# Optimization experiments

Measured on AMD Instinct MI355X. Metric: run time of the kernel, lower is better.

The kernel has to match this reference:

```python
import jax, jax.numpy as jnp
import numpy as np

B, H, T, D = 4, 16, 4096, 64
N_TASKS, K_LEN = 8, 128


def setup_inputs() -> dict:
    key = jax.random.key(0)
    ks = jax.random.split(key, 6)
    x = jax.random.normal(ks[0], (B, H, T, D), dtype=jnp.float32)
    q = jax.random.normal(ks[1], (B, H, T, D), dtype=jnp.float32)
    kv_k = jax.random.normal(ks[2], (N_TASKS, H, K_LEN, D), dtype=jnp.float32)
    kv_v = jax.random.normal(ks[3], (N_TASKS, H, K_LEN, D), dtype=jnp.float32)
    gates = jax.random.uniform(ks[4], (N_TASKS,), dtype=jnp.float32)
    trk_id = jax.random.randint(ks[5], (B, T), 0, N_TASKS, dtype=jnp.int64)
    return {"x": x, "q": q, "kv_k": kv_k, "kv_v": kv_v, "gates": gates, "trk_id": trk_id}


def reference(x, q, kv_k, kv_v, gates, trk_id):
    # Faithful to ICLAdaptor.fn: per-task SDPA of each token's query against
    # that task's (k, v) adaptor memory, scaled by a learned gate, scattered
    # back by trk_id, residual-added to x. Ragged torch gather/scatter is
    # expressed as masked per-task dense attention (small fixed n_tasks loop).
    d = q.shape[-1]
    scale = jnp.asarray(1.0, q.dtype) / jnp.sqrt(jnp.asarray(d, q.dtype))
    n_tasks = kv_k.shape[0]
    dx = jnp.zeros_like(q)
    for i in range(n_tasks):
        # scores: [b, h, t, k_len]
        s = jnp.einsum('bhtd,hkd->bhtk', q, kv_k[i]) * scale
        a = jax.nn.softmax(s, axis=-1)
        o = jnp.einsum('bhtk,hkd->bhtd', a, kv_v[i]) * gates[i]
        mask = (trk_id == i)[:, None, :, None]  # [b,1,t,1]
        dx = dx + jnp.where(mask, o, jnp.zeros((), o.dtype))
    return x + dx
```

## Files before the change

kernel.cpp:

```cpp
#include <hip/hip_runtime.h>

#define B_   4
#define H_   16
#define T_   4096
#define D_   64
#define KL_  128
#define NT_  8
#define NTOK (B_ * T_)
#define CAP  4096

typedef __bf16 bf16;
typedef __attribute__((ext_vector_type(8))) __bf16 bf16x8;
typedef __attribute__((ext_vector_type(4))) __bf16 bf16x4;
typedef __attribute__((ext_vector_type(4))) float  floatx4;


__global__ void zero_counts_k(int* __restrict__ ws) {
    if (threadIdx.x < NT_) ws[threadIdx.x] = 0;
}

__global__ void scatter_tokens_k(const int* __restrict__ trk, int* __restrict__ ws) {
    int* counts = ws;
    int* bucket = ws + NT_;
    int idx  = blockIdx.x * blockDim.x + threadIdx.x;
    int lane = threadIdx.x & 63;
    int task = (idx < NTOK) ? trk[idx] : -1;
    unsigned long long mymask = 0ull;
    int myCnt = 0;
#pragma unroll
    for (int i = 0; i < NT_; i++) {
        unsigned long long m = __ballot(task == i);
        if (task == i) mymask = m;
        if (lane == i) myCnt = (int)__popcll(m);
    }
    int b0 = 0;
    if (lane < NT_) b0 = atomicAdd(&counts[lane], myCnt);
    int myBase = __shfl(b0, (task < 0) ? 0 : task);
    if (idx < NTOK) {
        int pos = myBase + (int)__popcll(mymask & ((1ull << lane) - 1ull));
        bucket[task * CAP + pos] = idx;
    }
}

__global__ __launch_bounds__(256) void attn_k(
    const float* __restrict__ q,   const float* __restrict__ kvk,
    const float* __restrict__ kvv, const float* __restrict__ gates,
    const float* __restrict__ x,   float* __restrict__ out,
    const int* __restrict__ ws)
{
    __shared__ bf16 Kl[KL_ * 72];
    __shared__ bf16 Vt[D_ * 136];
    __shared__ bf16 Pl[4][16 * 136];

    const int task = blockIdx.z, h = blockIdx.y, chunk = blockIdx.x;
    const int cnt = ws[task];
    if (cnt == 0) return;
    const int* bucket = ws + NT_ + task * CAP;
    const float gate = gates[task];

    {
        const size_t kvbase = (size_t)(task * H_ + h) * (KL_ * D_ / 4);
        const float4* kf = (const float4*)kvk + kvbase;
        const float4* vf = (const float4*)kvv + kvbase;
        for (int ii = threadIdx.x; ii < KL_ * D_ / 4; ii += 256) {
            int k = ii >> 4, d4 = ii & 15;
            float4 a = kf[ii];
            bf16x4 w; w[0]=(bf16)a.x; w[1]=(bf16)a.y; w[2]=(bf16)a.z; w[3]=(bf16)a.w;
            *(bf16x4*)&Kl[k * 72 + d4 * 4] = w;
            float4 v = vf[ii];
            int d = d4 * 4;
            Vt[(d+0)*136 + k] = (bf16)v.x;
            Vt[(d+1)*136 + k] = (bf16)v.y;
            Vt[(d+2)*136 + k] = (bf16)v.z;
            Vt[(d+3)*136 + k] = (bf16)v.w;
        }
    }
    __syncthreads();

    const int wave = threadIdx.x >> 6;
    const int lane = threadIdx.x & 63;
    const int c = lane & 15, quad = lane >> 4;
    bf16* Pw = &Pl[wave][0];

    for (int ts = chunk * 4 + wave; ts * 16 < cnt; ts += 32) {
        int slotc = ts * 16 + c;
        int tokc  = bucket[slotc < cnt ? slotc : cnt - 1];
        int bb = tokc >> 12, tt = tokc & (T_ - 1);
        const float4* qf = (const float4*)q + ((size_t)((bb * H_ + h) * T_ + tt) * (D_ / 4));
        bf16x8 aq[2];
#pragma unroll
        for (int dc = 0; dc < 2; dc++) {
            float4 f0 = qf[dc * 8 + quad * 2];
            float4 f1 = qf[dc * 8 + quad * 2 + 1];
            aq[dc][0]=(bf16)f0.x; aq[dc][1]=(bf16)f0.y; aq[dc][2]=(bf16)f0.z; aq[dc][3]=(bf16)f0.w;
            aq[dc][4]=(bf16)f1.x; aq[dc][5]=(bf16)f1.y; aq[dc][6]=(bf16)f1.z; aq[dc][7]=(bf16)f1.w;
        }
        floatx4 sc[8];
#pragma unroll
        for (int nt = 0; nt < 8; nt++) {
            floatx4 z = {0.f, 0.f, 0.f, 0.f};
            sc[nt] = z;
#pragma unroll
            for (int dc = 0; dc < 2; dc++) {
                bf16x8 bk = *(const bf16x8*)&Kl[(nt * 16 + c) * 72 + dc * 32 + quad * 8];
                sc[nt] = __builtin_amdgcn_mfma_f32_16x16x32_bf16(aq[dc], bk, sc[nt], 0, 0, 0);
            }
        }
        float mx[4], lsum[4];
#pragma unroll
        for (int r = 0; r < 4; r++) {
            float m = -1e30f;
#pragma unroll
            for (int nt = 0; nt < 8; nt++) m = fmaxf(m, sc[nt][r]);
#pragma unroll
            for (int off = 1; off < 16; off <<= 1) m = fmaxf(m, __shfl_xor(m, off));
            mx[r] = m;
        }
#pragma unroll
        for (int r = 0; r < 4; r++) {
            float sum = 0.f;
#pragma unroll
            for (int nt = 0; nt < 8; nt++) {
                float p = exp2f((sc[nt][r] - mx[r]) * 0.18033688011112042f);
                sc[nt][r] = p;
                sum += p;
            }
#pragma unroll
            for (int off = 1; off < 16; off <<= 1) sum += __shfl_xor(sum, off);
            lsum[r] = sum;
        }
#pragma unroll
        for (int nt = 0; nt < 8; nt++)
#pragma unroll
            for (int r = 0; r < 4; r++)
                Pw[(quad * 4 + r) * 136 + nt * 16 + c] = (bf16)sc[nt][r];
        floatx4 acc[4];
#pragma unroll
        for (int dt = 0; dt < 4; dt++) { floatx4 z = {0.f,0.f,0.f,0.f}; acc[dt] = z; }
#pragma unroll
        for (int kc = 0; kc < 4; kc++) {
            bf16x8 ap = *(const bf16x8*)&Pw[c * 136 + kc * 32 + quad * 8];
#pragma unroll
            for (int dt = 0; dt < 4; dt++) {
                bf16x8 bv = *(const bf16x8*)&Vt[(dt * 16 + c) * 136 + kc * 32 + quad * 8];
                acc[dt] = __builtin_amdgcn_mfma_f32_16x16x32_bf16(ap, bv, acc[dt], 0, 0, 0);
            }
        }
#pragma unroll
        for (int r = 0; r < 4; r++) {
            int slot = ts * 16 + quad * 4 + r;
            if (slot < cnt) {
                int tok = bucket[slot];
                int b2 = tok >> 12, t2 = tok & (T_ - 1);
                float scale = gate / lsum[r];
                int base = ((b2 * H_ + h) * T_ + t2) * D_;
#pragma unroll
                for (int dt = 0; dt < 4; dt++) {
                    int off = base + dt * 16 + c;
                    out[off] = x[off] + acc[dt][r] * scale;
                }
            }
        }
    }
}

extern "C" void kernel_launch(void* const* d_in, const int* in_sizes, int n_in,
                              void* d_out, int out_size, void* d_ws, size_t ws_size,
                              hipStream_t stream) {
    const float* x     = (const float*)d_in[0];
    const float* q     = (const float*)d_in[1];
    const float* kvk   = (const float*)d_in[2];
    const float* kvv   = (const float*)d_in[3];
    const float* gates = (const float*)d_in[4];
    const int*   trk   = (const int*)d_in[5];
    float* out = (float*)d_out;
    int* ws = (int*)d_ws;

    zero_counts_k<<<1, 64, 0, stream>>>(ws);
    scatter_tokens_k<<<NTOK / 256, 256, 0, stream>>>(trk, ws);
    attn_k<<<dim3(8, H_, NT_), 256, 0, stream>>>(q, kvk, kvv, gates, x, out, ws);
}
```

Measured before the change: 239.9 us.

## Keep softmax probabilities in registers via shuffles and XOR-swizzle K/V LDS layout

Computes S transposed (K as the A operand) so each lane owns one token's scores. Softmax reductions then need only two cross-quad shuffles, and the P tile is rebuilt as the MFMA A operand through register shuffles instead of a per-wave LDS round trip. K and V^T in LDS switch from padded rows to XOR-swizzled unpadded rows to avoid bank conflicts. Other changes: x is prefetched before the matmuls, bucket reloads are replaced with shuffles, s_setprio is raised around the MFMA sections, and launch bounds now request 4 blocks per CU. The shuffle-based operand assembly adds VALU and cross-lane traffic in exchange for less LDS traffic and fewer syncs.

After: 271.1 us. +13.0%, slower.

```diff
diff --git a/kernel.cpp b/kernel.cpp
--- a/kernel.cpp
+++ b/kernel.cpp
@@ -13,7 +13,7 @@
 typedef __attribute__((ext_vector_type(8))) __bf16 bf16x8;
 typedef __attribute__((ext_vector_type(4))) __bf16 bf16x4;
 typedef __attribute__((ext_vector_type(4))) float  floatx4;
-
+typedef __attribute__((ext_vector_type(4))) unsigned int uint4v;
 
 __global__ void zero_counts_k(int* __restrict__ ws) {
     if (threadIdx.x < NT_) ws[threadIdx.x] = 0;
@@ -42,15 +42,20 @@
     }
 }
 
-__global__ __launch_bounds__(256) void attn_k(
+static __device__ __forceinline__ unsigned pk_bf16(float a, float b) {
+    unsigned short ua = __builtin_bit_cast(unsigned short, (bf16)a);
+    unsigned short ub = __builtin_bit_cast(unsigned short, (bf16)b);
+    return (unsigned)ua | ((unsigned)ub << 16);
+}
+
+__global__ __launch_bounds__(256, 4) void attn_k(
     const float* __restrict__ q,   const float* __restrict__ kvk,
     const float* __restrict__ kvv, const float* __restrict__ gates,
     const float* __restrict__ x,   float* __restrict__ out,
     const int* __restrict__ ws)
 {
-    __shared__ bf16 Kl[KL_ * 72];
-    __shared__ bf16 Vt[D_ * 136];
-    __shared__ bf16 Pl[4][16 * 136];
+    __shared__ bf16 Kl[KL_ * D_];
+    __shared__ bf16 Vt[D_ * KL_];
 
     const int task = blockIdx.z, h = blockIdx.y, chunk = blockIdx.x;
     const int cnt = ws[task];
@@ -62,102 +67,137 @@
         const size_t kvbase = (size_t)(task * H_ + h) * (KL_ * D_ / 4);
         const float4* kf = (const float4*)kvk + kvbase;
         const float4* vf = (const float4*)kvv + kvbase;
-        for (int ii = threadIdx.x; ii < KL_ * D_ / 4; ii += 256) {
+#pragma unroll
+        for (int it = 0; it < 8; it++) {
+            int ii = it * 256 + threadIdx.x;
             int k = ii >> 4, d4 = ii & 15;
             float4 a = kf[ii];
             bf16x4 w; w[0]=(bf16)a.x; w[1]=(bf16)a.y; w[2]=(bf16)a.z; w[3]=(bf16)a.w;
-            *(bf16x4*)&Kl[k * 72 + d4 * 4] = w;
+            *(bf16x4*)&Kl[(k << 6) + (((d4 >> 1) ^ (k & 7)) << 3) + ((d4 & 1) << 2)] = w;
             float4 v = vf[ii];
-            int d = d4 * 4;
-            Vt[(d+0)*136 + k] = (bf16)v.x;
-            Vt[(d+1)*136 + k] = (bf16)v.y;
-            Vt[(d+2)*136 + k] = (bf16)v.z;
-            Vt[(d+3)*136 + k] = (bf16)v.w;
+            int d0 = d4 << 2, ku = k >> 3, kl = k & 7;
+            Vt[(d0+0)*128 + ((ku ^ ((d0+0)&7))<<3) + kl] = (bf16)v.x;
+            Vt[(d0+1)*128 + ((ku ^ ((d0+1)&7))<<3) + kl] = (bf16)v.y;
+            Vt[(d0+2)*128 + ((ku ^ ((d0+2)&7))<<3) + kl] = (bf16)v.z;
+            Vt[(d0+3)*128 + ((ku ^ ((d0+3)&7))<<3) + kl] = (bf16)v.w;
         }
     }
     __syncthreads();
 
+    const int lane = threadIdx.x & 63;
     const int wave = threadIdx.x >> 6;
-    const int lane = threadIdx.x & 63;
     const int c = lane & 15, quad = lane >> 4;
-    bf16* Pw = &Pl[wave][0];
+    const int cswz = c & 7;
+    const int src_h0 = c + 16 * (( 2 * quad     ) & 3);
+    const int src_h1 = c + 16 * (( 2 * quad + 1 ) & 3);
+    const bool hiSel = ((quad >> 1) & 1) != 0;
 
     for (int ts = chunk * 4 + wave; ts * 16 < cnt; ts += 32) {
-        int slotc = ts * 16 + c;
-        int tokc  = bucket[slotc < cnt ? slotc : cnt - 1];
-        int bb = tokc >> 12, tt = tokc & (T_ - 1);
-        const float4* qf = (const float4*)q + ((size_t)((bb * H_ + h) * T_ + tt) * (D_ / 4));
+        const int slotc = ts * 16 + c;
+        const int tokc  = bucket[slotc < cnt ? slotc : cnt - 1];
+
         bf16x8 aq[2];
+        {
+            int bb = tokc >> 12, tt = tokc & (T_ - 1);
+            const float4* qf = (const float4*)q + ((size_t)((bb * H_ + h) * T_ + tt) * (D_ / 4));
+#pragma unroll
+            for (int dc = 0; dc < 2; dc++) {
+                float4 f0 = qf[dc * 8 + quad * 2];
+                float4 f1 = qf[dc * 8 + quad * 2 + 1];
+                aq[dc][0]=(bf16)f0.x; aq[dc][1]=(bf16)f0.y; aq[dc][2]=(bf16)f0.z; aq[dc][3]=(bf16)f0.w;
+                aq[dc][4]=(bf16)f1.x; aq[dc][5]=(bf16)f1.y; aq[dc][6]=(bf16)f1.z; aq[dc][7]=(bf16)f1.w;
+            }
+        }
+
+        float xr[4][4];
+        int base_r[4];
+#pragma unroll
+        for (int r = 0; r < 4; r++) {
+            int tok = __shfl(tokc, quad * 4 + r);
+            int b2 = tok >> 12, t2 = tok & (T_ - 1);
+            base_r[r] = ((b2 * H_ + h) * T_ + t2) * D_;
+            if (ts * 16 + quad * 4 + r < cnt) {
+#pragma unroll
+                for (int dt = 0; dt < 4; dt++) xr[r][dt] = x[base_r[r] + dt * 16 + c];
+            }
+        }
+
+        floatx4 sc[8];
+#pragma unroll
+        for (int nt = 0; nt < 8; nt++) { floatx4 z = {0.f,0.f,0.f,0.f}; sc[nt] = z; }
+        __builtin_amdgcn_s_setprio(1);
 #pragma unroll
         for (int dc = 0; dc < 2; dc++) {
-            float4 f0 = qf[dc * 8 + quad * 2];
-            float4 f1 = qf[dc * 8 + quad * 2 + 1];
-            aq[dc][0]=(bf16)f0.x; aq[dc][1]=(bf16)f0.y; aq[dc][2]=(bf16)f0.z; aq[dc][3]=(bf16)f0.w;
-            aq[dc][4]=(bf16)f1.x; aq[dc][5]=(bf16)f1.y; aq[dc][6]=(bf16)f1.z; aq[dc][7]=(bf16)f1.w;
-        }
-        floatx4 sc[8];
-#pragma unroll
-        for (int nt = 0; nt < 8; nt++) {
-            floatx4 z = {0.f, 0.f, 0.f, 0.f};
-            sc[nt] = z;
-#pragma unroll
-            for (int dc = 0; dc < 2; dc++) {
-                bf16x8 bk = *(const bf16x8*)&Kl[(nt * 16 + c) * 72 + dc * 32 + quad * 8];
-                sc[nt] = __builtin_amdgcn_mfma_f32_16x16x32_bf16(aq[dc], bk, sc[nt], 0, 0, 0);
-            }
-        }
-        float mx[4], lsum[4];
-#pragma unroll
-        for (int r = 0; r < 4; r++) {
-            float m = -1e30f;
-#pragma unroll
-            for (int nt = 0; nt < 8; nt++) m = fmaxf(m, sc[nt][r]);
-#pragma unroll
-            for (int off = 1; off < 16; off <<= 1) m = fmaxf(m, __shfl_xor(m, off));
-            mx[r] = m;
-        }
-#pragma unroll
-        for (int r = 0; r < 4; r++) {
-            float sum = 0.f;
 #pragma unroll
             for (int nt = 0; nt < 8; nt++) {
-                float p = exp2f((sc[nt][r] - mx[r]) * 0.18033688011112042f);
+                bf16x8 ak = *(const bf16x8*)&Kl[((nt * 16 + c) << 6) + (((4 * dc + quad) ^ cswz) << 3)];
+                sc[nt] = __builtin_amdgcn_mfma_f32_16x16x32_bf16(ak, aq[dc], sc[nt], 0, 0, 0);
+            }
+        }
+        __builtin_amdgcn_s_setprio(0);
+
+        float m = -1e30f;
+#pragma unroll
+        for (int nt = 0; nt < 8; nt++)
+#pragma unroll
+            for (int r = 0; r < 4; r++) m = fmaxf(m, sc[nt][r]);
+        m = fmaxf(m, __shfl_xor(m, 16));
+        m = fmaxf(m, __shfl_xor(m, 32));
+        float sum = 0.f;
+#pragma unroll
+        for (int nt = 0; nt < 8; nt++)
+#pragma unroll
+            for (int r = 0; r < 4; r++) {
+                float p = exp2f((sc[nt][r] - m) * 0.18033688011112042f);
                 sc[nt][r] = p;
                 sum += p;
             }
-#pragma unroll
-            for (int off = 1; off < 16; off <<= 1) sum += __shfl_xor(sum, off);
-            lsum[r] = sum;
-        }
-#pragma unroll
-        for (int nt = 0; nt < 8; nt++)
-#pragma unroll
-            for (int r = 0; r < 4; r++)
-                Pw[(quad * 4 + r) * 136 + nt * 16 + c] = (bf16)sc[nt][r];
+        sum += __shfl_xor(sum, 16);
+        sum += __shfl_xor(sum, 32);
+        float ginv = gate / sum;
+
+        unsigned pkv[8][2];
+#pragma unroll
+        for (int nt = 0; nt < 8; nt++) {
+            pkv[nt][0] = pk_bf16(sc[nt][0], sc[nt][1]);
+            pkv[nt][1] = pk_bf16(sc[nt][2], sc[nt][3]);
+        }
+
         floatx4 acc[4];
 #pragma unroll
         for (int dt = 0; dt < 4; dt++) { floatx4 z = {0.f,0.f,0.f,0.f}; acc[dt] = z; }
 #pragma unroll
         for (int kc = 0; kc < 4; kc++) {
-            bf16x8 ap = *(const bf16x8*)&Pw[c * 136 + kc * 32 + quad * 8];
+            unsigned e0 = pkv[2*kc][0],   e1 = pkv[2*kc][1];
+            unsigned o0 = pkv[2*kc+1][0], o1 = pkv[2*kc+1][1];
+            unsigned a0e = __shfl(e0, src_h0), a0o = __shfl(o0, src_h0);
+            unsigned a1e = __shfl(e1, src_h0), a1o = __shfl(o1, src_h0);
+            unsigned a2e = __shfl(e0, src_h1), a2o = __shfl(o0, src_h1);
+            unsigned a3e = __shfl(e1, src_h1), a3o = __shfl(o1, src_h1);
+            uint4v uw;
+            uw[0] = hiSel ? a0o : a0e;
+            uw[1] = hiSel ? a1o : a1e;
+            uw[2] = hiSel ? a2o : a2e;
+            uw[3] = hiSel ? a3o : a3e;
+            bf16x8 ap = __builtin_bit_cast(bf16x8, uw);
+            __builtin_amdgcn_s_setprio(1);
 #pragma unroll
             for (int dt = 0; dt < 4; dt++) {
-                bf16x8 bv = *(const bf16x8*)&Vt[(dt * 16 + c) * 136 + kc * 32 + quad * 8];
+                bf16x8 bv = *(const bf16x8*)&Vt[((dt * 16 + c) << 7) + (((4 * kc + quad) ^ cswz) << 3)];
                 acc[dt] = __builtin_amdgcn_mfma_f32_16x16x32_bf16(ap, bv, acc[dt], 0, 0, 0);
             }
-        }
+            __builtin_amdgcn_s_setprio(0);
+        }
+
 #pragma unroll
         for (int r = 0; r < 4; r++) {
             int slot = ts * 16 + quad * 4 + r;
+            float scale = __shfl(ginv, quad * 4 + r);
             if (slot < cnt) {
-                int tok = bucket[slot];
-                int b2 = tok >> 12, t2 = tok & (T_ - 1);
-                float scale = gate / lsum[r];
-                int base = ((b2 * H_ + h) * T_ + t2) * D_;
 #pragma unroll
                 for (int dt = 0; dt < 4; dt++) {
-                    int off = base + dt * 16 + c;
-                    out[off] = x[off] + acc[dt][r] * scale;
+                    int off = base_r[r] + dt * 16 + c;
+                    out[off] = xr[r][dt] + acc[dt][r] * scale;
                 }
             }
         }
```
